# Optimization experiments

Measured on AMD Instinct MI355X. Metric: run time of the kernel, lower is better.

Reference implementation:

```python
import jax, jax.numpy as jnp
import numpy as np

L, D, DM, H, FF = 2048, 32, 1024, 16, 4096
DH = DM // H  # 64
SCALE = float(np.sqrt(DH))


def layernorm(x, g, b, eps=1e-5):
    mu = jnp.mean(x, axis=-1, keepdims=True)
    var = jnp.mean(jnp.square(x - mu), axis=-1, keepdims=True)
    return (x - mu) * jax.lax.rsqrt(var + eps) * g + b


def setup_inputs() -> dict:
    key = jax.random.key(0)
    ks = jax.random.split(key, 8)
    p = lambda k, shp: jax.random.normal(k, shp, jnp.float32) * 0.02
    return {
        "src": jax.random.normal(ks[0], (L, DM), jnp.float32),
        "target": jax.random.normal(ks[1], (L, D, DM), jnp.float32),
        "attn_mask": jnp.zeros((L, D), jnp.float32),
        "Wq": p(ks[2], (DM, DM)), "bq": jnp.zeros((DM,), jnp.float32),
        "Wk": p(ks[3], (DM, DM)), "bk": jnp.zeros((DM,), jnp.float32),
        "Wv": p(ks[4], (DM, DM)), "bv": jnp.zeros((DM,), jnp.float32),
        "W1": p(ks[5], (DM, FF)), "b1": jnp.zeros((FF,), jnp.float32),
        "W2": p(ks[6], (FF, DM)), "b2": jnp.zeros((DM,), jnp.float32),
        "g1": jnp.ones((DM,), jnp.float32), "beta1": jnp.zeros((DM,), jnp.float32),
        "g2": jnp.ones((DM,), jnp.float32), "beta2": jnp.zeros((DM,), jnp.float32),
    }


def reference(src, target, attn_mask, Wq, bq, Wk, bk, Wv, bv,
              W1, b1, W2, b2, g1, beta1, g2, beta2):
    # projections: src (L, DM), target (L, D, DM)
    q = (src @ Wq + bq).reshape(L, H, DH)            # (L, H, DH)
    k = (target @ Wk + bk).reshape(L, D, H, DH)       # (L, D, H, DH)
    v = (target @ Wv + bv).reshape(L, D, H, DH)
    # per-position attention over the D candidates: scores (H, L, D)
    scores = jnp.einsum('lhd,lkhd->hlk', q, k) / SCALE
    scores = scores + attn_mask[None, :, :]
    probs = jax.nn.softmax(scores, axis=-1)
    ctx = jnp.einsum('hlk,lkhd->lhd', probs, v).reshape(L, DM)
    x = layernorm(src + ctx, g1, beta1)
    ff = jax.nn.gelu(x @ W1 + b1, approximate=False) @ W2 + b2
    return layernorm(x + ff, g2, beta2)
```

## Files before the change

kernel.cpp:

```cpp
#include <hip/hip_runtime.h>
#include <hip/hip_bf16.h>

#define L  2048
#define D  32
#define DM 1024
#define H  16
#define DH 64
#define FF 4096

typedef unsigned short u16;
typedef __attribute__((ext_vector_type(8))) short bf16x8;
typedef __attribute__((ext_vector_type(4))) float f32x4;
typedef __attribute__((ext_vector_type(4))) unsigned int u32x4;
typedef __attribute__((ext_vector_type(8))) unsigned short u16x8;
typedef __attribute__((ext_vector_type(4))) unsigned short u16x4;

static __device__ __forceinline__ float bf2f(u16 u) {
    return __uint_as_float(((unsigned)u) << 16);
}
static __device__ __forceinline__ u16 f2bf(float f) {
    union { __hip_bfloat16 b; u16 u; } cv;
    cv.b = __float2bfloat16(f);
    return cv.u;
}
static __device__ __forceinline__ void gll16(const u16* gsrc, u16* ldst) {
    __builtin_amdgcn_global_load_lds(
        (const __attribute__((address_space(1))) unsigned int*)gsrc,
        (__attribute__((address_space(3))) unsigned int*)ldst, 16, 0, 0);
}

__global__ __launch_bounds__(256) void cvt_bf(const float* __restrict__ in,
                                              u16* __restrict__ out, int n4) {
    int i = blockIdx.x * 256 + threadIdx.x;
    if (i < n4) {
        const float4 v = reinterpret_cast<const float4*>(in)[i];
        u16x4 o = { f2bf(v.x), f2bf(v.y), f2bf(v.z), f2bf(v.w) };
        *reinterpret_cast<u16x4*>(out + (long)i * 4) = o;
    }
}

__global__ void cvt_T(const float* __restrict__ in, u16* __restrict__ out, int R, int C) {
    __shared__ float tile[32][33];
    const int tx = threadIdx.x, ty = threadIdx.y;
    const int bx = blockIdx.x * 32, by = blockIdx.y * 32;
    #pragma unroll
    for (int i = 0; i < 32; i += 8)
        tile[ty + i][tx] = in[(long)(by + ty + i) * C + bx + tx];
    __syncthreads();
    #pragma unroll
    for (int i = 0; i < 32; i += 8)
        out[(long)(bx + ty + i) * R + by + tx] = f2bf(tile[tx][ty + i]);
}

#define LDT 40
template<int EPI>
__global__ __launch_bounds__(256) void gemm_bt(
    const u16* __restrict__ A, int lda, long aBS,
    const u16* __restrict__ Bt, int ldb, long bBS,
    void* __restrict__ Cv, int ldc, long cBS,
    const float* __restrict__ bias, int biasBS, int K)
{
    __shared__ u16 As[64 * LDT];
    __shared__ u16 Bs[64 * LDT];
    const int t = threadIdx.x;
    const int z = blockIdx.z;
    const int mBase = blockIdx.y * 64, nBase = blockIdx.x * 64;
    const u16* Ab = A + (long)z * aBS;
    const u16* Bb = Bt + (long)z * bBS;
    const int lane = t & 63, w = t >> 6;
    const int r = t >> 2, seg = t & 3;
    f32x4 acc[4] = { {0.f,0.f,0.f,0.f}, {0.f,0.f,0.f,0.f}, {0.f,0.f,0.f,0.f}, {0.f,0.f,0.f,0.f} };
    const long aRow = (long)(mBase + r) * lda;
    const long bRow = (long)(nBase + r) * ldb;
    for (int k0 = 0; k0 < K; k0 += 32) {
        __syncthreads();
        *reinterpret_cast<u32x4*>(&As[r * LDT + seg * 8]) =
            *reinterpret_cast<const u32x4*>(&Ab[aRow + k0 + seg * 8]);
        *reinterpret_cast<u32x4*>(&Bs[r * LDT + seg * 8]) =
            *reinterpret_cast<const u32x4*>(&Bb[bRow + k0 + seg * 8]);
        __syncthreads();
        const bf16x8 af = *reinterpret_cast<const bf16x8*>(
            &As[(w * 16 + (lane & 15)) * LDT + (lane >> 4) * 8]);
        #pragma unroll
        for (int j = 0; j < 4; ++j) {
            const bf16x8 bfr = *reinterpret_cast<const bf16x8*>(
                &Bs[(j * 16 + (lane & 15)) * LDT + (lane >> 4) * 8]);
            acc[j] = __builtin_amdgcn_mfma_f32_16x16x32_bf16(af, bfr, acc[j], 0, 0, 0);
        }
    }
    const int rbase = mBase + w * 16 + ((lane >> 4) << 2);
    const int cb = nBase + (lane & 15);
    #pragma unroll
    for (int j = 0; j < 4; ++j) {
        const int col = cb + j * 16;
        const float badd = bias ? bias[(long)z * biasBS + col] : 0.f;
        #pragma unroll
        for (int i = 0; i < 4; ++i) {
            float v = acc[j][i] + badd;
            if (EPI == 2) v = 0.5f * v * (1.f + erff(v * 0.70710678118654752f));
            const long off = (long)z * cBS + (long)(rbase + i) * ldc + col;
            if (EPI == 1) reinterpret_cast<float*>(Cv)[off] = v;
            else          reinterpret_cast<u16*>(Cv)[off]  = f2bf(v);
        }
    }
}

template<int EPI>
__global__ __launch_bounds__(256) void gemm128(
    const u16* __restrict__ A, int lda, long aZ,
    const u16* __restrict__ Bt, int ldb, long bZ,
    void* __restrict__ Cv, int ldc, long cZ,
    const float* __restrict__ bias, int K)
{
    __shared__ u16 As[128 * 64];
    __shared__ u16 Bs[128 * 64];
    const int t = threadIdx.x, lane = t & 63, w = t >> 6;
    const int z = blockIdx.z;
    const int mBase = blockIdx.y * 128, nBase = blockIdx.x * 128;
    const u16* Ab = A + (long)z * aZ;
    const u16* Bb = Bt + (long)z * bZ;
    const int wr = w >> 1, wc = w & 1;
    const int sr = lane >> 3, sg = lane & 7, sswz = sg ^ sr;
    f32x4 acc[4][4];
    #pragma unroll
    for (int mi = 0; mi < 4; ++mi)
        #pragma unroll
        for (int ni = 0; ni < 4; ++ni) acc[mi][ni] = (f32x4){0.f, 0.f, 0.f, 0.f};

    for (int k0 = 0; k0 < K; k0 += 64) {
        #pragma unroll
        for (int i = 0; i < 4; ++i) {
            const int r = w * 32 + i * 8 + sr;
            gll16(&Ab[(long)(mBase + r) * lda + k0 + sswz * 8], &As[r * 64 + sg * 8]);
        }
        #pragma unroll
        for (int i = 0; i < 4; ++i) {
            const int r = w * 32 + i * 8 + sr;
            gll16(&Bb[(long)(nBase + r) * ldb + k0 + sswz * 8], &Bs[r * 64 + sg * 8]);
        }
        __syncthreads();
        #pragma unroll
        for (int ks = 0; ks < 2; ++ks) {
            bf16x8 aF[4], bF[4];
            #pragma unroll
            for (int mi = 0; mi < 4; ++mi) {
                const int rr = wr * 64 + mi * 16 + (lane & 15);
                aF[mi] = *reinterpret_cast<const bf16x8*>(
                    &As[rr * 64 + ((ks * 4 + (lane >> 4)) ^ (rr & 7)) * 8]);
            }
            #pragma unroll
            for (int ni = 0; ni < 4; ++ni) {
                const int rr = wc * 64 + ni * 16 + (lane & 15);
                bF[ni] = *reinterpret_cast<const bf16x8*>(
                    &Bs[rr * 64 + ((ks * 4 + (lane >> 4)) ^ (rr & 7)) * 8]);
            }
            #pragma unroll
            for (int mi = 0; mi < 4; ++mi)
                #pragma unroll
                for (int ni = 0; ni < 4; ++ni)
                    acc[mi][ni] = __builtin_amdgcn_mfma_f32_16x16x32_bf16(
                        aF[mi], bF[ni], acc[mi][ni], 0, 0, 0);
        }
        __syncthreads();
    }
    const int rb = mBase + wr * 64 + ((lane >> 4) << 2);
    const int cb = nBase + wc * 64 + (lane & 15);
    #pragma unroll
    for (int mi = 0; mi < 4; ++mi) {
        #pragma unroll
        for (int ni = 0; ni < 4; ++ni) {
            const int col = cb + ni * 16;
            const float badd = bias ? bias[col] : 0.f;
            #pragma unroll
            for (int i = 0; i < 4; ++i) {
                float v = acc[mi][ni][i] + badd;
                if (EPI == 2) v = 0.5f * v * (1.f + erff(v * 0.70710678118654752f));
                const long off = (long)z * cZ + (long)(rb + mi * 16 + i) * ldc + col;
                if (EPI == 1) reinterpret_cast<float*>(Cv)[off] = v;
                else          reinterpret_cast<u16*>(Cv)[off]  = f2bf(v);
            }
        }
    }
}

#define NL 8
template<bool QKLDS>
__global__ __launch_bounds__(512) void attn_mfma(
    const u16* __restrict__ qk,
    const float* __restrict__ target,
    const float* __restrict__ mask,
    u16* __restrict__ tw)
{
    extern __shared__ u16 smem[];
    u16* tgtS = smem;
    u16* qkS  = smem + D * DM;

    const int t = threadIdx.x, lane = t & 63, w = t >> 6;
    const int g = lane >> 4, hm = lane & 15;
    const int l0 = blockIdx.x * NL;

    float4 pf[16];
    u16x8  qf[4];
    {
        const float* tl = target + (long)l0 * (D * DM);
        #pragma unroll
        for (int it = 0; it < 16; ++it)
            pf[it] = reinterpret_cast<const float4*>(tl)[it * 512 + t];
        if (QKLDS) {
            const u16* ql = qk + (long)l0 * (H * DM);
            #pragma unroll
            for (int it = 0; it < 4; ++it)
                qf[it] = reinterpret_cast<const u16x8*>(ql)[it * 512 + t];
        }
    }

    for (int li = 0; li < NL; ++li) {
        const int l = l0 + li;
        #pragma unroll
        for (int it = 0; it < 16; ++it) {
            const int i = it * 512 + t;
            const int d = i >> 8, mm = (i & 255) * 4, cc = mm ^ ((d & 15) << 3);
            u16x4 o = { f2bf(pf[it].x), f2bf(pf[it].y), f2bf(pf[it].z), f2bf(pf[it].w) };
            *reinterpret_cast<u16x4*>(&tgtS[d * DM + cc]) = o;
        }
        if (QKLDS) {
            #pragma unroll
            for (int it = 0; it < 4; ++it) {
                const int i = it * 512 + t;
                const int h = i >> 7, mm = (i & 127) * 8, cc = mm ^ ((h & 15) << 3);
                *reinterpret_cast<u16x8*>(&qkS[h * DM + cc]) = qf[it];
            }
        }
        const float* mrow = mask + (long)l * D;
        float mk[8];
        #pragma unroll
        for (int r = 0; r < 4; ++r) { mk[r] = mrow[4 * g + r]; mk[4 + r] = mrow[16 + 4 * g + r]; }
        __syncthreads();

        if constexpr (QKLDS) {
            if (li < NL - 1) {
                const float* tn = target + (long)(l + 1) * (D * DM);
                #pragma unroll
                for (int it = 0; it < 16; ++it)
                    pf[it] = reinterpret_cast<const float4*>(tn)[it * 512 + t];
                const u16* qn = qk + (long)(l + 1) * (H * DM);
                #pragma unroll
                for (int it = 0; it < 4; ++it)
                    qf[it] = reinterpret_cast<const u16x8*>(qn)[it * 512 + t];
            }
        }

        f32x4 acc0 = {0.f, 0.f, 0.f, 0.f}, acc1 = {0.f, 0.f, 0.f, 0.f};
        const u16* qrow = qk + (long)l * (H * DM) + hm * DM;
        const int swz = hm << 3;
        #pragma unroll 4
        for (int ks = 0; ks < 32; ++ks) {
            const int mcol = ks * 32 + g * 8;
            bf16x8 yf;
            if (QKLDS) yf = *reinterpret_cast<const bf16x8*>(&qkS[hm * DM + (mcol ^ swz)]);
            else       yf = *reinterpret_cast<const bf16x8*>(&qrow[mcol]);
            const bf16x8 x0 = *reinterpret_cast<const bf16x8*>(&tgtS[hm * DM + (mcol ^ swz)]);
            const bf16x8 x1 = *reinterpret_cast<const bf16x8*>(&tgtS[(16 + hm) * DM + (mcol ^ swz)]);
            acc0 = __builtin_amdgcn_mfma_f32_16x16x32_bf16(x0, yf, acc0, 0, 0, 0);
            acc1 = __builtin_amdgcn_mfma_f32_16x16x32_bf16(x1, yf, acc1, 0, 0, 0);
        }

        if constexpr (!QKLDS) {
            if (li < NL - 1) {
                const float* tn = target + (long)(l + 1) * (D * DM);
                #pragma unroll
                for (int it = 0; it < 16; ++it)
                    pf[it] = reinterpret_cast<const float4*>(tn)[it * 512 + t];
            }
        }

        float sc[8];
        #pragma unroll
        for (int r = 0; r < 4; ++r) {
            sc[r]     = acc0[r] * 0.125f + mk[r];
            sc[4 + r] = acc1[r] * 0.125f + mk[4 + r];
        }
        float mx = sc[0];
        #pragma unroll
        for (int r = 1; r < 8; ++r) mx = fmaxf(mx, sc[r]);
        mx = fmaxf(mx, __shfl_xor(mx, 16));
        mx = fmaxf(mx, __shfl_xor(mx, 32));
        float sum = 0.f;
        #pragma unroll
        for (int r = 0; r < 8; ++r) { sc[r] = __expf(sc[r] - mx); sum += sc[r]; }
        sum += __shfl_xor(sum, 16);
        sum += __shfl_xor(sum, 32);
        const float pinv = 1.0f / sum;
        bf16x8 pfrag;
        #pragma unroll
        for (int r = 0; r < 8; ++r) pfrag[r] = (short)f2bf(sc[r] * pinv);

        u16* twl = tw + (long)l * (H * DM);
        const f32x4 zero = {0.f, 0.f, 0.f, 0.f};
        #pragma unroll
        for (int i = 0; i < 8; ++i) {
            const int mg = w * 8 + i;
            const int m = mg * 16 + hm;
            bf16x8 af;
            #pragma unroll
            for (int j = 0; j < 4; ++j) {
                const int d0 = 4 * g + j;
                const int d1 = 16 + 4 * g + j;
                af[j]     = (short)tgtS[d0 * DM + (m ^ (d0 << 3))];
                af[4 + j] = (short)tgtS[d1 * DM + (m ^ (d0 << 3))];
            }
            const f32x4 c = __builtin_amdgcn_mfma_f32_16x16x32_bf16(af, pfrag, zero, 0, 0, 0);
            u16x4 o = { f2bf(c[0]), f2bf(c[1]), f2bf(c[2]), f2bf(c[3]) };
            *reinterpret_cast<u16x4*>(&twl[hm * DM + mg * 16 + 4 * g]) = o;
        }
        __syncthreads();
    }
}

__global__ __launch_bounds__(256) void ln_fuse(
    const float* __restrict__ a, const float* __restrict__ b,
    const float* __restrict__ c, const float* __restrict__ bvec,
    const float* __restrict__ g, const float* __restrict__ be,
    float* __restrict__ o32, u16* __restrict__ o16)
{
    const int l = blockIdx.x, t = threadIdx.x;
    __shared__ float S[4], SS[4];
    __shared__ float stats[2];
    const float4 va = reinterpret_cast<const float4*>(a + (long)l * DM)[t];
    const float4 vb = reinterpret_cast<const float4*>(b + (long)l * DM)[t];
    float v[4] = { va.x + vb.x, va.y + vb.y, va.z + vb.z, va.w + vb.w };
    if (c) {
        const float4 vc = reinterpret_cast<const float4*>(c + (long)l * DM)[t];
        v[0] += vc.x; v[1] += vc.y; v[2] += vc.z; v[3] += vc.w;
    }
    if (bvec) {
        const float4 vv = reinterpret_cast<const float4*>(bvec)[t];
        v[0] += vv.x; v[1] += vv.y; v[2] += vv.z; v[3] += vv.w;
    }
    float s  = v[0] + v[1] + v[2] + v[3];
    float ss = v[0]*v[0] + v[1]*v[1] + v[2]*v[2] + v[3]*v[3];
    #pragma unroll
    for (int off = 32; off; off >>= 1) { s += __shfl_down(s, off); ss += __shfl_down(ss, off); }
    if ((t & 63) == 0) { S[t >> 6] = s; SS[t >> 6] = ss; }
    __syncthreads();
    if (t == 0) {
        const float St  = S[0] + S[1] + S[2] + S[3];
        const float SSt = SS[0] + SS[1] + SS[2] + SS[3];
        const float mu  = St * (1.f / DM);
        const float var = fmaxf(SSt * (1.f / DM) - mu * mu, 0.f);
        stats[0] = mu;
        stats[1] = rsqrtf(var + 1e-5f);
    }
    __syncthreads();
    const float mu = stats[0], rs = stats[1];
    const int c0 = t * 4;
    float ov[4];
    #pragma unroll
    for (int j = 0; j < 4; ++j) ov[j] = (v[j] - mu) * rs * g[c0 + j] + be[c0 + j];
    float4 o; o.x = ov[0]; o.y = ov[1]; o.z = ov[2]; o.w = ov[3];
    reinterpret_cast<float4*>(o32 + (long)l * DM)[t] = o;
    if (o16) {
        u16x4 q = { f2bf(ov[0]), f2bf(ov[1]), f2bf(ov[2]), f2bf(ov[3]) };
        *reinterpret_cast<u16x4*>(o16 + (long)l * DM + c0) = q;
    }
}

extern "C" void kernel_launch(void* const* d_in, const int* in_sizes, int n_in,
                              void* d_out, int out_size, void* d_ws, size_t ws_size,
                              hipStream_t stream)
{
    const float* src    = (const float*)d_in[0];
    const float* target = (const float*)d_in[1];
    const float* amask  = (const float*)d_in[2];
    const float* Wq = (const float*)d_in[3];
    const float* bq = (const float*)d_in[4];
    const float* Wk = (const float*)d_in[5];
    const float* Wv = (const float*)d_in[7];
    const float* bv = (const float*)d_in[8];
    const float* W1 = (const float*)d_in[9];
    const float* b1 = (const float*)d_in[10];
    const float* W2 = (const float*)d_in[11];
    const float* b2 = (const float*)d_in[12];
    const float* g1  = (const float*)d_in[13];
    const float* be1 = (const float*)d_in[14];
    const float* g2  = (const float*)d_in[15];
    const float* be2 = (const float*)d_in[16];

    char* ws = (char*)d_ws;
    const size_t MB = (size_t)1 << 20;
    u16*   src16 = (u16*)  (ws +  0 * MB);
    u16*   Wk16  = (u16*)  (ws +  4 * MB);
    u16*   WqT   = (u16*)  (ws +  6 * MB);
    u16*   WvT   = (u16*)  (ws +  8 * MB);
    u16*   W1T   = (u16*)  (ws + 10 * MB);
    u16*   W2T   = (u16*)  (ws + 18 * MB);
    u16*   Q16   = (u16*)  (ws + 26 * MB);
    u16*   qk16  = (u16*)  (ws + 30 * MB);
    u16*   Y16   = (u16*)  (ws + 30 * MB);
    float* Z32   = (float*)(ws + 46 * MB);
    float* Z32b  = Z32 + (long)L * DM;
    float* ctx32 = (float*)(ws + 54 * MB);
    float* x32   = (float*)(ws + 62 * MB);
    u16*   x16   = (u16*)  (ws + 70 * MB);
    u16*   tw16  = (u16*)  (ws + 94 * MB);

    cvt_bf<<<2048, 256, 0, stream>>>(src, src16, (L * DM) / 4);
    cvt_bf<<<1024, 256, 0, stream>>>(Wk, Wk16, (DM * DM) / 4);
    dim3 tb(32, 8);
    cvt_T<<<dim3(32, 32),  tb, 0, stream>>>(Wq, WqT, DM, DM);
    cvt_T<<<dim3(32, 32),  tb, 0, stream>>>(Wv, WvT, DM, DM);
    cvt_T<<<dim3(128, 32), tb, 0, stream>>>(W1, W1T, DM, FF);
    cvt_T<<<dim3(32, 128), tb, 0, stream>>>(W2, W2T, FF, DM);

    gemm_bt<0><<<dim3(DM / 64, L / 64, 1), 256, 0, stream>>>(
        src16, DM, 0, WqT, DM, 0, Q16, DM, 0, bq, 0, DM);
    gemm_bt<0><<<dim3(DM / 64, L / 64, H), 256, 0, stream>>>(
        Q16, DM, DH, Wk16, DM, DH, qk16, H * DM, DM, nullptr, 0, DH);

    (void)hipGetLastError();
    (void)hipFuncSetAttribute(reinterpret_cast<const void*>(&attn_mfma<true>),
                              hipFuncAttributeMaxDynamicSharedMemorySize, 96 * 1024);
    attn_mfma<true><<<L / NL, 512, 96 * 1024, stream>>>(qk16, target, amask, tw16);
    if (hipGetLastError() != hipSuccess) {
        attn_mfma<false><<<L / NL, 512, 64 * 1024, stream>>>(qk16, target, amask, tw16);
    }

    gemm_bt<1><<<dim3(1, L / 64, H), 256, 0, stream>>>(
        tw16, H * DM, DM, WvT, DM, (long)DH * DM, ctx32, DM, DH, bv, DH, DM);
    ln_fuse<<<L, 256, 0, stream>>>(src, ctx32, nullptr, nullptr, g1, be1, x32, x16);
    gemm128<2><<<dim3(FF / 128, L / 128, 1), 256, 0, stream>>>(
        x16, DM, 0, W1T, DM, 0, Y16, FF, 0, b1, DM);
    gemm128<1><<<dim3(DM / 128, L / 128, 2), 256, 0, stream>>>(
        Y16, FF, 2048, W2T, FF, 2048, Z32, DM, (long)L * DM, nullptr, 2048);
    ln_fuse<<<L, 256, 0, stream>>>(x32, Z32, Z32b, b2, g2, be2, (float*)d_out, nullptr);
}
```

Before: 298.6 us.

## Merge prep kernels, replace small GEMMs with gemm128, double-buffer attention

The six conversion and transpose launches are merged into two multiplexed kernels. The 64-tile gemm_bt kernels are replaced by a gemm128 template with a configurable N tile and per-z bias. The attention kernel now double-buffers the target tiles in LDS and splits the QK reduction across the 8 waves with an LDS reduction, holding q fragments in registers. The aim is to cut launch overhead, use the faster tiled GEMM, and overlap global loads with compute, at the cost of 144KB of LDS per block and an extra reduction sync per position.

```diff
diff --git a/kernel.cpp b/kernel.cpp
--- a/kernel.cpp
+++ b/kernel.cpp
@@ -15,9 +15,6 @@
 typedef __attribute__((ext_vector_type(8))) unsigned short u16x8;
 typedef __attribute__((ext_vector_type(4))) unsigned short u16x4;
 
-static __device__ __forceinline__ float bf2f(u16 u) {
-    return __uint_as_float(((unsigned)u) << 16);
-}
 static __device__ __forceinline__ u16 f2bf(float f) {
     union { __hip_bfloat16 b; u16 u; } cv;
     cv.b = __float2bfloat16(f);
@@ -29,20 +26,30 @@
         (__attribute__((address_space(3))) unsigned int*)ldst, 16, 0, 0);
 }
 
-__global__ __launch_bounds__(256) void cvt_bf(const float* __restrict__ in,
-                                              u16* __restrict__ out, int n4) {
-    int i = blockIdx.x * 256 + threadIdx.x;
-    if (i < n4) {
-        const float4 v = reinterpret_cast<const float4*>(in)[i];
-        u16x4 o = { f2bf(v.x), f2bf(v.y), f2bf(v.z), f2bf(v.w) };
-        *reinterpret_cast<u16x4*>(out + (long)i * 4) = o;
-    }
-}
-
-__global__ void cvt_T(const float* __restrict__ in, u16* __restrict__ out, int R, int C) {
+__global__ __launch_bounds__(256) void prep_bf(const float* __restrict__ a, u16* __restrict__ oa,
+                                               const float* __restrict__ b, u16* __restrict__ ob) {
+    const int i = blockIdx.x * 256 + threadIdx.x;
+    const int na4 = (L * DM) / 4;
+    const float* in;  u16* out;  int j;
+    if (i < na4) { in = a; out = oa; j = i; }
+    else         { in = b; out = ob; j = i - na4; }
+    const float4 v = reinterpret_cast<const float4*>(in)[j];
+    u16x4 o = { f2bf(v.x), f2bf(v.y), f2bf(v.z), f2bf(v.w) };
+    *reinterpret_cast<u16x4*>(out + (long)j * 4) = o;
+}
+
+__global__ void prep_T(const float* __restrict__ Wq, u16* __restrict__ oWq,
+                       const float* __restrict__ Wv, u16* __restrict__ oWv,
+                       const float* __restrict__ W1, u16* __restrict__ oW1,
+                       const float* __restrict__ W2, u16* __restrict__ oW2) {
     __shared__ float tile[32][33];
+    const int b = blockIdx.x;
+    const float* in; u16* out; int R, C, bx, by;
+    if (b < 1024)      { in = Wq; out = oWq; R = DM; C = DM; int bb = b;        bx = (bb & 31) * 32;  by = (bb >> 5) * 32; }
+    else if (b < 2048) { in = Wv; out = oWv; R = DM; C = DM; int bb = b - 1024; bx = (bb & 31) * 32;  by = (bb >> 5) * 32; }
+    else if (b < 6144) { in = W1; out = oW1; R = DM; C = FF; int bb = b - 2048; bx = (bb & 127) * 32; by = (bb >> 7) * 32; }
+    else               { in = W2; out = oW2; R = FF; C = DM; int bb = b - 6144; bx = (bb & 31) * 32;  by = (bb >> 5) * 32; }
     const int tx = threadIdx.x, ty = threadIdx.y;
-    const int bx = blockIdx.x * 32, by = blockIdx.y * 32;
     #pragma unroll
     for (int i = 0; i < 32; i += 8)
         tile[ty + i][tx] = in[(long)(by + ty + i) * C + bx + tx];
@@ -52,80 +59,28 @@
         out[(long)(bx + ty + i) * R + by + tx] = f2bf(tile[tx][ty + i]);
 }
 
-#define LDT 40
-template<int EPI>
-__global__ __launch_bounds__(256) void gemm_bt(
-    const u16* __restrict__ A, int lda, long aBS,
-    const u16* __restrict__ Bt, int ldb, long bBS,
-    void* __restrict__ Cv, int ldc, long cBS,
-    const float* __restrict__ bias, int biasBS, int K)
-{
-    __shared__ u16 As[64 * LDT];
-    __shared__ u16 Bs[64 * LDT];
-    const int t = threadIdx.x;
-    const int z = blockIdx.z;
-    const int mBase = blockIdx.y * 64, nBase = blockIdx.x * 64;
-    const u16* Ab = A + (long)z * aBS;
-    const u16* Bb = Bt + (long)z * bBS;
-    const int lane = t & 63, w = t >> 6;
-    const int r = t >> 2, seg = t & 3;
-    f32x4 acc[4] = { {0.f,0.f,0.f,0.f}, {0.f,0.f,0.f,0.f}, {0.f,0.f,0.f,0.f}, {0.f,0.f,0.f,0.f} };
-    const long aRow = (long)(mBase + r) * lda;
-    const long bRow = (long)(nBase + r) * ldb;
-    for (int k0 = 0; k0 < K; k0 += 32) {
-        __syncthreads();
-        *reinterpret_cast<u32x4*>(&As[r * LDT + seg * 8]) =
-            *reinterpret_cast<const u32x4*>(&Ab[aRow + k0 + seg * 8]);
-        *reinterpret_cast<u32x4*>(&Bs[r * LDT + seg * 8]) =
-            *reinterpret_cast<const u32x4*>(&Bb[bRow + k0 + seg * 8]);
-        __syncthreads();
-        const bf16x8 af = *reinterpret_cast<const bf16x8*>(
-            &As[(w * 16 + (lane & 15)) * LDT + (lane >> 4) * 8]);
-        #pragma unroll
-        for (int j = 0; j < 4; ++j) {
-            const bf16x8 bfr = *reinterpret_cast<const bf16x8*>(
-                &Bs[(j * 16 + (lane & 15)) * LDT + (lane >> 4) * 8]);
-            acc[j] = __builtin_amdgcn_mfma_f32_16x16x32_bf16(af, bfr, acc[j], 0, 0, 0);
-        }
-    }
-    const int rbase = mBase + w * 16 + ((lane >> 4) << 2);
-    const int cb = nBase + (lane & 15);
-    #pragma unroll
-    for (int j = 0; j < 4; ++j) {
-        const int col = cb + j * 16;
-        const float badd = bias ? bias[(long)z * biasBS + col] : 0.f;
-        #pragma unroll
-        for (int i = 0; i < 4; ++i) {
-            float v = acc[j][i] + badd;
-            if (EPI == 2) v = 0.5f * v * (1.f + erff(v * 0.70710678118654752f));
-            const long off = (long)z * cBS + (long)(rbase + i) * ldc + col;
-            if (EPI == 1) reinterpret_cast<float*>(Cv)[off] = v;
-            else          reinterpret_cast<u16*>(Cv)[off]  = f2bf(v);
-        }
-    }
-}
-
-template<int EPI>
+template<int EPI, int BN>
 __global__ __launch_bounds__(256) void gemm128(
     const u16* __restrict__ A, int lda, long aZ,
     const u16* __restrict__ Bt, int ldb, long bZ,
     void* __restrict__ Cv, int ldc, long cZ,
-    const float* __restrict__ bias, int K)
+    const float* __restrict__ bias, int biasZ, int K)
 {
+    constexpr int NI = BN / 32;
     __shared__ u16 As[128 * 64];
-    __shared__ u16 Bs[128 * 64];
+    __shared__ u16 Bs[BN * 64];
     const int t = threadIdx.x, lane = t & 63, w = t >> 6;
     const int z = blockIdx.z;
-    const int mBase = blockIdx.y * 128, nBase = blockIdx.x * 128;
+    const int mBase = blockIdx.y * 128, nBase = blockIdx.x * BN;
     const u16* Ab = A + (long)z * aZ;
     const u16* Bb = Bt + (long)z * bZ;
     const int wr = w >> 1, wc = w & 1;
     const int sr = lane >> 3, sg = lane & 7, sswz = sg ^ sr;
-    f32x4 acc[4][4];
+    f32x4 acc[4][NI];
     #pragma unroll
     for (int mi = 0; mi < 4; ++mi)
         #pragma unroll
-        for (int ni = 0; ni < 4; ++ni) acc[mi][ni] = (f32x4){0.f, 0.f, 0.f, 0.f};
+        for (int ni = 0; ni < NI; ++ni) acc[mi][ni] = (f32x4){0.f, 0.f, 0.f, 0.f};
 
     for (int k0 = 0; k0 < K; k0 += 64) {
         #pragma unroll
@@ -134,14 +89,14 @@
             gll16(&Ab[(long)(mBase + r) * lda + k0 + sswz * 8], &As[r * 64 + sg * 8]);
         }
         #pragma unroll
-        for (int i = 0; i < 4; ++i) {
-            const int r = w * 32 + i * 8 + sr;
+        for (int i = 0; i < NI; ++i) {
+            const int r = w * (BN / 4) + i * 8 + sr;
             gll16(&Bb[(long)(nBase + r) * ldb + k0 + sswz * 8], &Bs[r * 64 + sg * 8]);
         }
         __syncthreads();
         #pragma unroll
         for (int ks = 0; ks < 2; ++ks) {
-            bf16x8 aF[4], bF[4];
+            bf16x8 aF[4], bF[NI];
             #pragma unroll
             for (int mi = 0; mi < 4; ++mi) {
                 const int rr = wr * 64 + mi * 16 + (lane & 15);
@@ -149,28 +104,28 @@
                     &As[rr * 64 + ((ks * 4 + (lane >> 4)) ^ (rr & 7)) * 8]);
             }
             #pragma unroll
-            for (int ni = 0; ni < 4; ++ni) {
-                const int rr = wc * 64 + ni * 16 + (lane & 15);
+            for (int ni = 0; ni < NI; ++ni) {
+                const int rr = wc * (BN / 2) + ni * 16 + (lane & 15);
                 bF[ni] = *reinterpret_cast<const bf16x8*>(
                     &Bs[rr * 64 + ((ks * 4 + (lane >> 4)) ^ (rr & 7)) * 8]);
             }
             #pragma unroll
             for (int mi = 0; mi < 4; ++mi)
                 #pragma unroll
-                for (int ni = 0; ni < 4; ++ni)
+                for (int ni = 0; ni < NI; ++ni)
                     acc[mi][ni] = __builtin_amdgcn_mfma_f32_16x16x32_bf16(
                         aF[mi], bF[ni], acc[mi][ni], 0, 0, 0);
         }
         __syncthreads();
     }
     const int rb = mBase + wr * 64 + ((lane >> 4) << 2);
-    const int cb = nBase + wc * 64 + (lane & 15);
+    const int cb = nBase + wc * (BN / 2) + (lane & 15);
     #pragma unroll
     for (int mi = 0; mi < 4; ++mi) {
         #pragma unroll
-        for (int ni = 0; ni < 4; ++ni) {
+        for (int ni = 0; ni < NI; ++ni) {
             const int col = cb + ni * 16;
-            const float badd = bias ? bias[col] : 0.f;
+            const float badd = bias ? bias[(long)z * biasZ + col] : 0.f;
             #pragma unroll
             for (int i = 0; i < 4; ++i) {
                 float v = acc[mi][ni][i] + badd;
@@ -183,102 +138,105 @@
     }
 }
 
-#define NL 8
-template<bool QKLDS>
-__global__ __launch_bounds__(512) void attn_mfma(
+#define NLV5 8
+__global__ __launch_bounds__(512, 2) void attn_v5(
     const u16* __restrict__ qk,
     const float* __restrict__ target,
     const float* __restrict__ mask,
     u16* __restrict__ tw)
 {
     extern __shared__ u16 smem[];
-    u16* tgtS = smem;
-    u16* qkS  = smem + D * DM;
+    u16*   tgtS0 = smem;
+    u16*   tgtS1 = smem + D * DM;
+    f32x4* red   = (f32x4*)(smem + 2 * D * DM);
 
     const int t = threadIdx.x, lane = t & 63, w = t >> 6;
     const int g = lane >> 4, hm = lane & 15;
-    const int l0 = blockIdx.x * NL;
+    const int l0 = blockIdx.x * NLV5;
 
     float4 pf[16];
-    u16x8  qf[4];
+    bf16x8 qc[2][4];
     {
         const float* tl = target + (long)l0 * (D * DM);
         #pragma unroll
         for (int it = 0; it < 16; ++it)
             pf[it] = reinterpret_cast<const float4*>(tl)[it * 512 + t];
-        if (QKLDS) {
-            const u16* ql = qk + (long)l0 * (H * DM);
-            #pragma unroll
-            for (int it = 0; it < 4; ++it)
-                qf[it] = reinterpret_cast<const u16x8*>(ql)[it * 512 + t];
-        }
-    }
-
-    for (int li = 0; li < NL; ++li) {
-        const int l = l0 + li;
         #pragma unroll
         for (int it = 0; it < 16; ++it) {
             const int i = it * 512 + t;
             const int d = i >> 8, mm = (i & 255) * 4, cc = mm ^ ((d & 15) << 3);
             u16x4 o = { f2bf(pf[it].x), f2bf(pf[it].y), f2bf(pf[it].z), f2bf(pf[it].w) };
-            *reinterpret_cast<u16x4*>(&tgtS[d * DM + cc]) = o;
-        }
-        if (QKLDS) {
-            #pragma unroll
-            for (int it = 0; it < 4; ++it) {
-                const int i = it * 512 + t;
-                const int h = i >> 7, mm = (i & 127) * 8, cc = mm ^ ((h & 15) << 3);
-                *reinterpret_cast<u16x8*>(&qkS[h * DM + cc]) = qf[it];
-            }
-        }
+            *reinterpret_cast<u16x4*>(&tgtS0[d * DM + cc]) = o;
+        }
+        const float* tn = target + (long)(l0 + 1) * (D * DM);
+        #pragma unroll
+        for (int it = 0; it < 16; ++it)
+            pf[it] = reinterpret_cast<const float4*>(tn)[it * 512 + t];
+        const u16* qb = qk + (long)l0 * (H * DM) + hm * DM + w * 128 + g * 8;
+        #pragma unroll
+        for (int ks = 0; ks < 4; ++ks)
+            qc[0][ks] = *reinterpret_cast<const bf16x8*>(&qb[ks * 32]);
+    }
+    __syncthreads();
+
+    #pragma unroll
+    for (int li = 0; li < NLV5; ++li) {
+        const int l = l0 + li;
+        const int cur = li & 1, nxt = cur ^ 1;
+        u16* curS = cur ? tgtS1 : tgtS0;
+        u16* nxtS = cur ? tgtS0 : tgtS1;
+
         const float* mrow = mask + (long)l * D;
         float mk[8];
         #pragma unroll
         for (int r = 0; r < 4; ++r) { mk[r] = mrow[4 * g + r]; mk[4 + r] = mrow[16 + 4 * g + r]; }
-        __syncthreads();
-
-        if constexpr (QKLDS) {
-            if (li < NL - 1) {
-                const float* tn = target + (long)(l + 1) * (D * DM);
+
+        if (li < NLV5 - 1) {
+            #pragma unroll
+            for (int it = 0; it < 16; ++it) {
+                const int i = it * 512 + t;
+                const int d = i >> 8, mm = (i & 255) * 4, cc = mm ^ ((d & 15) << 3);
+                u16x4 o = { f2bf(pf[it].x), f2bf(pf[it].y), f2bf(pf[it].z), f2bf(pf[it].w) };
+                *reinterpret_cast<u16x4*>(&nxtS[d * DM + cc]) = o;
+            }
+            if (li < NLV5 - 2) {
+                const float* tn = target + (long)(l + 2) * (D * DM);
                 #pragma unroll
                 for (int it = 0; it < 16; ++it)
                     pf[it] = reinterpret_cast<const float4*>(tn)[it * 512 + t];
-                const u16* qn = qk + (long)(l + 1) * (H * DM);
-                #pragma unroll
-                for (int it = 0; it < 4; ++it)
-                    qf[it] = reinterpret_cast<const u16x8*>(qn)[it * 512 + t];
-            }
-        }
-
-        f32x4 acc0 = {0.f, 0.f, 0.f, 0.f}, acc1 = {0.f, 0.f, 0.f, 0.f};
-        const u16* qrow = qk + (long)l * (H * DM) + hm * DM;
+            }
+            const u16* qn = qk + (long)(l + 1) * (H * DM) + hm * DM + w * 128 + g * 8;
+            #pragma unroll
+            for (int ks = 0; ks < 4; ++ks)
+                qc[nxt][ks] = *reinterpret_cast<const bf16x8*>(&qn[ks * 32]);
+        }
+
+        f32x4 a0 = {0.f, 0.f, 0.f, 0.f}, a1 = {0.f, 0.f, 0.f, 0.f};
         const int swz = hm << 3;
-        #pragma unroll 4
-        for (int ks = 0; ks < 32; ++ks) {
-            const int mcol = ks * 32 + g * 8;
-            bf16x8 yf;
-            if (QKLDS) yf = *reinterpret_cast<const bf16x8*>(&qkS[hm * DM + (mcol ^ swz)]);
-            else       yf = *reinterpret_cast<const bf16x8*>(&qrow[mcol]);
-            const bf16x8 x0 = *reinterpret_cast<const bf16x8*>(&tgtS[hm * DM + (mcol ^ swz)]);
-            const bf16x8 x1 = *reinterpret_cast<const bf16x8*>(&tgtS[(16 + hm) * DM + (mcol ^ swz)]);
-            acc0 = __builtin_amdgcn_mfma_f32_16x16x32_bf16(x0, yf, acc0, 0, 0, 0);
-            acc1 = __builtin_amdgcn_mfma_f32_16x16x32_bf16(x1, yf, acc1, 0, 0, 0);
-        }
-
-        if constexpr (!QKLDS) {
-            if (li < NL - 1) {
-                const float* tn = target + (long)(l + 1) * (D * DM);
-                #pragma unroll
-                for (int it = 0; it < 16; ++it)
-                    pf[it] = reinterpret_cast<const float4*>(tn)[it * 512 + t];
-            }
+        #pragma unroll
+        for (int ks = 0; ks < 4; ++ks) {
+            const int mcol = w * 128 + ks * 32 + g * 8;
+            const bf16x8 x0 = *reinterpret_cast<const bf16x8*>(&curS[hm * DM + (mcol ^ swz)]);
+            const bf16x8 x1 = *reinterpret_cast<const bf16x8*>(&curS[(16 + hm) * DM + (mcol ^ swz)]);
+            a0 = __builtin_amdgcn_mfma_f32_16x16x32_bf16(x0, qc[cur][ks], a0, 0, 0, 0);
+            a1 = __builtin_amdgcn_mfma_f32_16x16x32_bf16(x1, qc[cur][ks], a1, 0, 0, 0);
+        }
+        red[(w * 2 + 0) * 64 + lane] = a0;
+        red[(w * 2 + 1) * 64 + lane] = a1;
+        __syncthreads();
+
+        f32x4 s0 = red[lane], s1 = red[64 + lane];
+        #pragma unroll
+        for (int ww = 1; ww < 8; ++ww) {
+            s0 += red[(ww * 2 + 0) * 64 + lane];
+            s1 += red[(ww * 2 + 1) * 64 + lane];
         }
 
         float sc[8];
         #pragma unroll
         for (int r = 0; r < 4; ++r) {
-            sc[r]     = acc0[r] * 0.125f + mk[r];
-            sc[4 + r] = acc1[r] * 0.125f + mk[4 + r];
+            sc[r]     = s0[r] * 0.125f + mk[r];
+            sc[4 + r] = s1[r] * 0.125f + mk[4 + r];
         }
         float mx = sc[0];
         #pragma unroll
@@ -306,8 +264,8 @@
             for (int j = 0; j < 4; ++j) {
                 const int d0 = 4 * g + j;
                 const int d1 = 16 + 4 * g + j;
-                af[j]     = (short)tgtS[d0 * DM + (m ^ (d0 << 3))];
-                af[4 + j] = (short)tgtS[d1 * DM + (m ^ (d0 << 3))];
+                af[j]     = (short)curS[d0 * DM + (m ^ (d0 << 3))];
+                af[4 + j] = (short)curS[d1 * DM + (m ^ (d0 << 3))];
             }
             const f32x4 c = __builtin_amdgcn_mfma_f32_16x16x32_bf16(af, pfrag, zero, 0, 0, 0);
             u16x4 o = { f2bf(c[0]), f2bf(c[1]), f2bf(c[2]), f2bf(c[3]) };
@@ -404,33 +362,24 @@
     u16*   x16   = (u16*)  (ws + 70 * MB);
     u16*   tw16  = (u16*)  (ws + 94 * MB);
 
-    cvt_bf<<<2048, 256, 0, stream>>>(src, src16, (L * DM) / 4);
-    cvt_bf<<<1024, 256, 0, stream>>>(Wk, Wk16, (DM * DM) / 4);
-    dim3 tb(32, 8);
-    cvt_T<<<dim3(32, 32),  tb, 0, stream>>>(Wq, WqT, DM, DM);
-    cvt_T<<<dim3(32, 32),  tb, 0, stream>>>(Wv, WvT, DM, DM);
-    cvt_T<<<dim3(128, 32), tb, 0, stream>>>(W1, W1T, DM, FF);
-    cvt_T<<<dim3(32, 128), tb, 0, stream>>>(W2, W2T, FF, DM);
-
-    gemm_bt<0><<<dim3(DM / 64, L / 64, 1), 256, 0, stream>>>(
+    prep_bf<<<3072, 256, 0, stream>>>(src, src16, Wk, Wk16);
+    prep_T<<<10240, dim3(32, 8), 0, stream>>>(Wq, WqT, Wv, WvT, W1, W1T, W2, W2T);
+
+    gemm128<0, 128><<<dim3(DM / 128, L / 128, 1), 256, 0, stream>>>(
         src16, DM, 0, WqT, DM, 0, Q16, DM, 0, bq, 0, DM);
-    gemm_bt<0><<<dim3(DM / 64, L / 64, H), 256, 0, stream>>>(
+    gemm128<0, 128><<<dim3(DM / 128, L / 128, H), 256, 0, stream>>>(
         Q16, DM, DH, Wk16, DM, DH, qk16, H * DM, DM, nullptr, 0, DH);
 
-    (void)hipGetLastError();
-    (void)hipFuncSetAttribute(reinterpret_cast<const void*>(&attn_mfma<true>),
-                              hipFuncAttributeMaxDynamicSharedMemorySize, 96 * 1024);
-    attn_mfma<true><<<L / NL, 512, 96 * 1024, stream>>>(qk16, target, amask, tw16);
-    if (hipGetLastError() != hipSuccess) {
-        attn_mfma<false><<<L / NL, 512, 64 * 1024, stream>>>(qk16, target, amask, tw16);
-    }
-
-    gemm_bt<1><<<dim3(1, L / 64, H), 256, 0, stream>>>(
+    (void)hipFuncSetAttribute(reinterpret_cast<const void*>(&attn_v5),
+                              hipFuncAttributeMaxDynamicSharedMemorySize, 144 * 1024);
+    attn_v5<<<L / NLV5, 512, 144 * 1024, stream>>>(qk16, target, amask, tw16);
+
+    gemm128<1, 64><<<dim3(1, L / 128, H), 256, 0, stream>>>(
         tw16, H * DM, DM, WvT, DM, (long)DH * DM, ctx32, DM, DH, bv, DH, DM);
     ln_fuse<<<L, 256, 0, stream>>>(src, ctx32, nullptr, nullptr, g1, be1, x32, x16);
-    gemm128<2><<<dim3(FF / 128, L / 128, 1), 256, 0, stream>>>(
-        x16, DM, 0, W1T, DM, 0, Y16, FF, 0, b1, DM);
-    gemm128<1><<<dim3(DM / 128, L / 128, 2), 256, 0, stream>>>(
-        Y16, FF, 2048, W2T, FF, 2048, Z32, DM, (long)L * DM, nullptr, 2048);
+    gemm128<2, 128><<<dim3(FF / 128, L / 128, 1), 256, 0, stream>>>(
+        x16, DM, 0, W1T, DM, 0, Y16, FF, 0, b1, 0, DM);
+    gemm128<1, 128><<<dim3(DM / 128, L / 128, 2), 256, 0, stream>>>(
+        Y16, FF, 2048, W2T, FF, 2048, Z32, DM, (long)L * DM, nullptr, 0, 2048);
     ln_fuse<<<L, 256, 0, stream>>>(x32, Z32, Z32b, b2, g2, be2, (float*)d_out, nullptr);
 }
```

Result: faster. 278.4 us (-6.8%).
